# Kernel tuning notes

Hardware: AMD Instinct MI355X
Metric: run time of the kernel (lower is better)

Reference implementation:

```python
import jax, jax.numpy as jnp
import numpy as np

EMBED_DIM = 1024
HEAD_DIM = 64
BATCH = 2
SEQ = 4096


def setup_inputs() -> dict:
    key = jax.random.key(0)
    kx, kq, kk, kv = jax.random.split(key, 4)
    x = jax.random.normal(kx, (BATCH, SEQ, EMBED_DIM), dtype=jnp.float32)
    # nn.Linear(embedding_dim, head_dim, bias=False) weights, stored as [in, out]
    s = 1.0 / np.sqrt(EMBED_DIM)
    Wq = jax.random.uniform(kq, (EMBED_DIM, HEAD_DIM), jnp.float32, -s, s)
    Wk = jax.random.uniform(kk, (EMBED_DIM, HEAD_DIM), jnp.float32, -s, s)
    Wv = jax.random.uniform(kv, (EMBED_DIM, HEAD_DIM), jnp.float32, -s, s)
    return {"x": x, "Wq": Wq, "Wk": Wk, "Wv": Wv}


def reference(x, Wq, Wk, Wv):
    # x: [B, S, E]
    Q = x @ Wq  # [B, S, D]
    K = x @ Wk
    V = x @ Wv
    seq_len = Q.shape[1]
    head_dim = Q.shape[2]
    scores = jnp.einsum('bsd,btd->bst', Q, K) / jnp.sqrt(jnp.float32(head_dim))
    # Original adds a mask that is 1.0 on the causal (lower-tri) positions and
    # -inf elsewhere (tril(ones) with zeros replaced by -inf). The +1 on allowed
    # positions is a uniform row shift, but we keep it for bitwise faithfulness.
    causal = jnp.tril(jnp.ones((seq_len, seq_len), dtype=scores.dtype))
    mask = jnp.where(causal == 0, -jnp.inf, causal)
    scores = scores + mask  # [B, S, S]
    attn = jax.nn.softmax(scores, axis=-1)
    return jnp.einsum('bst,btd->bsd', attn, V)  # [B, S, D]
```

## Files before the change

### kernel.cpp

```cpp
#include <hip/hip_runtime.h>
#include <hip/hip_bf16.h>


typedef short short8 __attribute__((ext_vector_type(8)));
typedef float f32x4 __attribute__((ext_vector_type(4)));
typedef float f32x16 __attribute__((ext_vector_type(16)));
typedef unsigned int uint4e __attribute__((ext_vector_type(4)));
typedef unsigned short ushort4e __attribute__((ext_vector_type(4)));

#define NEGINF (-3.0e38f)
#define SCQ 0.18033688011112042f

static __device__ __forceinline__ unsigned short f2bf(float f) {
  __hip_bfloat16 h = __float2bfloat16(f);
  return __builtin_bit_cast(unsigned short, h);
}

static __device__ __forceinline__ f32x16 mfma32(short8 a, short8 b, f32x16 c) {
  return __builtin_amdgcn_mfma_f32_32x32x16_bf16(a, b, c, 0, 0, 0);
}

__global__ __launch_bounds__(256) void wprep_kernel(
    const float* __restrict__ Wq, const float* __restrict__ Wk,
    const float* __restrict__ Wv, unsigned short* __restrict__ Wt) {
  int w = blockIdx.x >> 3;
  int kc = blockIdx.x & 7;
  int k0 = kc * 128;
  const float* W = (w == 0) ? Wq : ((w == 1) ? Wk : Wv);
  float sc = (w == 0) ? SCQ : 1.0f;

  __shared__ unsigned short lt[128][66];
#pragma unroll
  for (int i = 0; i < 32; ++i) {
    int e = i * 256 + threadIdx.x;
    int k = e >> 6, n = e & 63;
    lt[k][n] = f2bf(W[(size_t)(k0 + k) * 64 + n] * sc);
  }
  __syncthreads();
#pragma unroll
  for (int i = 0; i < 32; ++i) {
    int e = i * 256 + threadIdx.x;
    int n = e >> 7, k = e & 127;
    Wt[(size_t)(w * 64 + n) * 1024 + k0 + k] = lt[k][n];
  }
}

__global__ __launch_bounds__(256, 2) void qkv_proj_kernel(
    const float* __restrict__ x, const unsigned short* __restrict__ Wt,
    unsigned short* __restrict__ Qb, unsigned short* __restrict__ Kb,
    unsigned short* __restrict__ Vt) {
  int lane = threadIdx.x & 63;
  int w = threadIdx.x >> 6;
  int r = lane & 15;
  int hi = lane >> 4;
  int sbase = blockIdx.x * 16;

  __shared__ alignas(16) float lds_part[4][3072];

  const float* xp = x + (size_t)(sbase + r) * 1024 + w * 256 + hi * 8;

  f32x4 acc[12];
#pragma unroll
  for (int t = 0; t < 12; ++t)
#pragma unroll
    for (int i = 0; i < 4; ++i) acc[t][i] = 0.f;

  f32x4 a0 = *(const f32x4*)(xp);
  f32x4 a1 = *(const f32x4*)(xp + 4);
#pragma unroll
  for (int k0 = 0; k0 < 256; k0 += 32) {
    short8 af;
#pragma unroll
    for (int j = 0; j < 4; ++j) {
      af[j] = (short)f2bf(a0[j]);
      af[4 + j] = (short)f2bf(a1[j]);
    }
    if (k0 + 32 < 256) {
      a0 = *(const f32x4*)(xp + k0 + 32);
      a1 = *(const f32x4*)(xp + k0 + 36);
    }
    const unsigned short* wb = Wt + (size_t)r * 1024 + w * 256 + k0 + hi * 8;
#pragma unroll
    for (int t = 0; t < 12; ++t) {
      short8 bf = *(const short8*)(wb + (size_t)((t >> 2) * 64 + (t & 3) * 16) * 1024);
      acc[t] = __builtin_amdgcn_mfma_f32_16x16x32_bf16(af, bf, acc[t], 0, 0, 0);
    }
  }

  float* lp = lds_part[w];
#pragma unroll
  for (int t = 0; t < 12; ++t)
#pragma unroll
    for (int v = 0; v < 4; ++v)
      lp[t * 256 + (hi * 4 + v) * 16 + r] = acc[t][v];
  __syncthreads();

#pragma unroll
  for (int i = 0; i < 2; ++i) {
    int task = threadIdx.x + i * 256;
    int t = task >> 6;
    int off = (task & 63) * 4;
    f32x4 s = *(const f32x4*)(&lds_part[0][t * 256 + off]);
    s += *(const f32x4*)(&lds_part[1][t * 256 + off]);
    s += *(const f32x4*)(&lds_part[2][t * 256 + off]);
    s += *(const f32x4*)(&lds_part[3][t * 256 + off]);
    int row = off >> 4, c0 = off & 15;
    ushort4e pk;
#pragma unroll
    for (int j = 0; j < 4; ++j) pk[j] = f2bf(s[j]);
    unsigned short* dst = (t < 4) ? Qb : Kb;
    *(ushort4e*)(dst + (size_t)(sbase + row) * 64 + (t & 3) * 16 + c0) = pk;
  }
  {
    int t = 8 + (threadIdx.x >> 6);
    int col = (threadIdx.x >> 2) & 15;
    int rg = threadIdx.x & 3;
    ushort4e pk;
#pragma unroll
    for (int j = 0; j < 4; ++j) {
      int idx = t * 256 + (rg * 4 + j) * 16 + col;
      float s = lds_part[0][idx] + lds_part[1][idx] + lds_part[2][idx] + lds_part[3][idx];
      pk[j] = f2bf(s);
    }
    int d = (t - 8) * 16 + col;
    int bidx = sbase >> 12, so = sbase & 4095;
    *(ushort4e*)(Vt + ((size_t)(bidx * 64 + d)) * 4096 + so + rg * 4) = pk;
  }
}

__global__ __launch_bounds__(512, 2) void attn_kernel(
    const unsigned short* __restrict__ Qb, const unsigned short* __restrict__ Kb,
    const unsigned short* __restrict__ Vt, float* __restrict__ out) {
  int qglob = blockIdx.x;
  int b = qglob >> 7;
  int q = qglob & 127;
  int lane = threadIdx.x & 63;
  int p = threadIdx.x >> 6;
  int ql = lane & 31;
  int h = lane >> 5;
  int sbase = q * 32;

  __shared__ float sm[8][32];
  __shared__ float sl[8][32];
  __shared__ alignas(16) float Op[8][32][68];

  const unsigned short* Qp = Qb + ((size_t)(b * 4096 + sbase + ql)) * 64 + h * 8;
  short8 qf0 = *(const short8*)(Qp);
  short8 qf1 = *(const short8*)(Qp + 16);
  short8 qf2 = *(const short8*)(Qp + 32);
  short8 qf3 = *(const short8*)(Qp + 48);

  f32x16 o0, o1;
#pragma unroll
  for (int i = 0; i < 16; ++i) { o0[i] = 0.f; o1[i] = 0.f; }
  float m = NEGINF, l = 0.f;

  int npairs = (q + 2) >> 1;
  const unsigned short* Kbb = Kb + (size_t)b * 4096 * 64;
  const unsigned short* Vbb = Vt + ((size_t)(b * 64 + ql)) * 4096 + h * 8;

  short8 k0a, k0b, k0c, k0d, k1a, k1b, k1c, k1d;
  {
    const unsigned short* Kp = Kbb + (size_t)(p * 64 + ql) * 64 + h * 8;
    k0a = *(const short8*)(Kp);
    k0b = *(const short8*)(Kp + 16);
    k0c = *(const short8*)(Kp + 32);
    k0d = *(const short8*)(Kp + 48);
    k1a = *(const short8*)(Kp + 2048);
    k1b = *(const short8*)(Kp + 2048 + 16);
    k1c = *(const short8*)(Kp + 2048 + 32);
    k1d = *(const short8*)(Kp + 2048 + 48);
  }

  for (int j = p; j < npairs; j += 8) {
    int kbase = j * 64;
    const unsigned short* Vp = Vbb + kbase;
    short8 vf0 = *(const short8*)(Vp);
    short8 vf1 = *(const short8*)(Vp + 16);
    short8 vf2 = *(const short8*)(Vp + 32);
    short8 vf3 = *(const short8*)(Vp + 48);
    short8 vg0 = *(const short8*)(Vp + 32 * 4096);
    short8 vg1 = *(const short8*)(Vp + 32 * 4096 + 16);
    short8 vg2 = *(const short8*)(Vp + 32 * 4096 + 32);
    short8 vg3 = *(const short8*)(Vp + 32 * 4096 + 48);

    f32x16 st0, st1;
#pragma unroll
    for (int i = 0; i < 16; ++i) { st0[i] = 0.f; st1[i] = 0.f; }
    st0 = mfma32(k0a, qf0, st0);
    st0 = mfma32(k0b, qf1, st0);
    st0 = mfma32(k0c, qf2, st0);
    st0 = mfma32(k0d, qf3, st0);
    st1 = mfma32(k1a, qf0, st1);
    st1 = mfma32(k1b, qf1, st1);
    st1 = mfma32(k1c, qf2, st1);
    st1 = mfma32(k1d, qf3, st1);

    if (j + 8 < npairs) {
      const unsigned short* Kp = Kbb + (size_t)((j + 8) * 64 + ql) * 64 + h * 8;
      k0a = *(const short8*)(Kp);
      k0b = *(const short8*)(Kp + 16);
      k0c = *(const short8*)(Kp + 32);
      k0d = *(const short8*)(Kp + 48);
      k1a = *(const short8*)(Kp + 2048);
      k1b = *(const short8*)(Kp + 2048 + 16);
      k1c = *(const short8*)(Kp + 2048 + 32);
      k1d = *(const short8*)(Kp + 2048 + 48);
    }

    if (2 * j == q) {
#pragma unroll
      for (int rg = 0; rg < 16; ++rg) {
        int kvl = (rg & 3) + 8 * (rg >> 2) + 4 * h;
        if (kvl > ql) st0[rg] = NEGINF;
        st1[rg] = NEGINF;
      }
    } else if (2 * j + 1 == q) {
#pragma unroll
      for (int rg = 0; rg < 16; ++rg) {
        int kvl = (rg & 3) + 8 * (rg >> 2) + 4 * h;
        if (kvl > ql) st1[rg] = NEGINF;
      }
    }

    float mx[16];
#pragma unroll
    for (int i = 0; i < 16; ++i) mx[i] = fmaxf(st0[i], st1[i]);
#pragma unroll
    for (int s = 8; s >= 1; s >>= 1)
#pragma unroll
      for (int i = 0; i < s; ++i) mx[i] = fmaxf(mx[i], mx[i + s]);
    float tm = fmaxf(mx[0], __shfl_xor(mx[0], 32));
    float nm = fmaxf(m, tm);
    float alpha = exp2f(m - nm);
#pragma unroll
    for (int i = 0; i < 16; ++i) {
      st0[i] = exp2f(st0[i] - nm);
      st1[i] = exp2f(st1[i] - nm);
    }
    float sv[16];
#pragma unroll
    for (int i = 0; i < 16; ++i) sv[i] = st0[i] + st1[i];
#pragma unroll
    for (int s = 8; s >= 1; s >>= 1)
#pragma unroll
      for (int i = 0; i < s; ++i) sv[i] += sv[i + s];
    float sum = sv[0] + __shfl_xor(sv[0], 32);
    l = l * alpha + sum;
    m = nm;
#pragma unroll
    for (int i = 0; i < 16; ++i) { o0[i] *= alpha; o1[i] *= alpha; }

    unsigned int pw0[8], pw1[8], sw0[8], sw1[8];
#pragma unroll
    for (int t = 0; t < 8; ++t) {
      pw0[t] = (unsigned int)f2bf(st0[2 * t]) | ((unsigned int)f2bf(st0[2 * t + 1]) << 16);
      pw1[t] = (unsigned int)f2bf(st1[2 * t]) | ((unsigned int)f2bf(st1[2 * t + 1]) << 16);
    }
#pragma unroll
    for (int t = 0; t < 8; ++t) {
      sw0[t] = __shfl_xor(pw0[t], 32);
      sw1[t] = __shfl_xor(pw1[t], 32);
    }
    uint4e bw0 = {h ? sw0[2] : pw0[0], h ? sw0[3] : pw0[1], h ? pw0[2] : sw0[0], h ? pw0[3] : sw0[1]};
    uint4e bw1 = {h ? sw0[6] : pw0[4], h ? sw0[7] : pw0[5], h ? pw0[6] : sw0[4], h ? pw0[7] : sw0[5]};
    uint4e bw2 = {h ? sw1[2] : pw1[0], h ? sw1[3] : pw1[1], h ? pw1[2] : sw1[0], h ? pw1[3] : sw1[1]};
    uint4e bw3 = {h ? sw1[6] : pw1[4], h ? sw1[7] : pw1[5], h ? pw1[6] : sw1[4], h ? pw1[7] : sw1[5]};
    short8 pb0 = __builtin_bit_cast(short8, bw0);
    short8 pb1 = __builtin_bit_cast(short8, bw1);
    short8 pb2 = __builtin_bit_cast(short8, bw2);
    short8 pb3 = __builtin_bit_cast(short8, bw3);

    o0 = mfma32(vf0, pb0, o0);
    o0 = mfma32(vf1, pb1, o0);
    o0 = mfma32(vf2, pb2, o0);
    o0 = mfma32(vf3, pb3, o0);
    o1 = mfma32(vg0, pb0, o1);
    o1 = mfma32(vg1, pb1, o1);
    o1 = mfma32(vg2, pb2, o1);
    o1 = mfma32(vg3, pb3, o1);
  }

  if (h == 0) sm[p][ql] = m;
  __syncthreads();
  float gm = sm[0][ql];
#pragma unroll
  for (int i = 1; i < 8; ++i) gm = fmaxf(gm, sm[i][ql]);
  float alpha = exp2f(m - gm);
  if (h == 0) sl[p][ql] = alpha * l;
  float* Ob = &Op[p][ql][0];
#pragma unroll
  for (int u = 0; u < 4; ++u) {
    f32x4 w0 = {alpha * o0[4 * u], alpha * o0[4 * u + 1], alpha * o0[4 * u + 2], alpha * o0[4 * u + 3]};
    *(f32x4*)(Ob + u * 8 + h * 4) = w0;
    f32x4 w1 = {alpha * o1[4 * u], alpha * o1[4 * u + 1], alpha * o1[4 * u + 2], alpha * o1[4 * u + 3]};
    *(f32x4*)(Ob + 32 + u * 8 + h * 4) = w1;
  }
  __syncthreads();

  int row = threadIdx.x >> 4;
  int c4 = (threadIdx.x & 15) * 4;
  f32x4 accv = *(const f32x4*)(&Op[0][row][c4]);
#pragma unroll
  for (int pp = 1; pp < 8; ++pp) accv += *(const f32x4*)(&Op[pp][row][c4]);
  float lsum = sl[0][row];
#pragma unroll
  for (int pp = 1; pp < 8; ++pp) lsum += sl[pp][row];
  float invl = 1.0f / lsum;
  f32x4 res;
#pragma unroll
  for (int j = 0; j < 4; ++j) res[j] = accv[j] * invl;
  *(f32x4*)(out + ((size_t)(b * 4096 + sbase + row)) * 64 + c4) = res;
}

extern "C" void kernel_launch(void* const* d_in, const int* in_sizes, int n_in,
                              void* d_out, int out_size, void* d_ws, size_t ws_size,
                              hipStream_t stream) {
  const float* x  = (const float*)d_in[0];
  const float* Wq = (const float*)d_in[1];
  const float* Wk = (const float*)d_in[2];
  const float* Wv = (const float*)d_in[3];
  float* out = (float*)d_out;

  if (ws_size < 3538944) return;

  char* ws = (char*)d_ws;
  unsigned short* Wt = (unsigned short*)(ws + 0);
  unsigned short* Qb = (unsigned short*)(ws + 393216);
  unsigned short* Kb = (unsigned short*)(ws + 1441792);
  unsigned short* Vt = (unsigned short*)(ws + 2490368);

  wprep_kernel<<<24, 256, 0, stream>>>(Wq, Wk, Wv, Wt);
  qkv_proj_kernel<<<512, 256, 0, stream>>>(x, Wt, Qb, Kb, Vt);
  attn_kernel<<<256, 512, 0, stream>>>(Qb, Kb, Vt, out);
}
```

Baseline: 134.1 us.

## Split attention KV range across four blocks with a separate combine kernel

The attention kernel now launches 1024 blocks of 256 threads instead of 256 blocks of 512. Each q-tile's KV pairs are split across four blocks (16 wave-groups total), and block order is reversed so the heaviest causal tiles run first. Partial outputs, maxes and sums go to workspace, and a new combine kernel merges them. The goal is better load balance and GPU occupancy on the causal workload. It adds an extra kernel launch plus about 8 MB of partial writes and reads. s_setprio hints are also placed around the MFMA blocks.

```diff
diff --git a/kernel.cpp b/kernel.cpp
--- a/kernel.cpp
+++ b/kernel.cpp
@@ -15,7 +15,6 @@
   __hip_bfloat16 h = __float2bfloat16(f);
   return __builtin_bit_cast(unsigned short, h);
 }
-
 static __device__ __forceinline__ f32x16 mfma32(short8 a, short8 b, f32x16 c) {
   return __builtin_amdgcn_mfma_f32_32x32x16_bf16(a, b, c, 0, 0, 0);
 }
@@ -128,21 +127,24 @@
   }
 }
 
-__global__ __launch_bounds__(512, 2) void attn_kernel(
+__global__ __launch_bounds__(256, 2) void attn_kernel(
     const unsigned short* __restrict__ Qb, const unsigned short* __restrict__ Kb,
-    const unsigned short* __restrict__ Vt, float* __restrict__ out) {
-  int qglob = blockIdx.x;
-  int b = qglob >> 7;
-  int q = qglob & 127;
+    const unsigned short* __restrict__ Vt, float* __restrict__ Opart,
+    float* __restrict__ Mpart, float* __restrict__ Lpart) {
+  int bid = blockIdx.x;
+  int q = 127 - (bid >> 3);
+  int b = (bid >> 2) & 1;
+  int hh = bid & 3;
   int lane = threadIdx.x & 63;
   int p = threadIdx.x >> 6;
+  int g = hh * 4 + p;
   int ql = lane & 31;
   int h = lane >> 5;
   int sbase = q * 32;
 
-  __shared__ float sm[8][32];
-  __shared__ float sl[8][32];
-  __shared__ alignas(16) float Op[8][32][68];
+  __shared__ float sm[4][32];
+  __shared__ float sl[4][32];
+  __shared__ alignas(16) float Op[4][32][68];
 
   const unsigned short* Qp = Qb + ((size_t)(b * 4096 + sbase + ql)) * 64 + h * 8;
   short8 qf0 = *(const short8*)(Qp);
@@ -161,7 +163,7 @@
 
   short8 k0a, k0b, k0c, k0d, k1a, k1b, k1c, k1d;
   {
-    const unsigned short* Kp = Kbb + (size_t)(p * 64 + ql) * 64 + h * 8;
+    const unsigned short* Kp = Kbb + (size_t)(g * 64 + ql) * 64 + h * 8;
     k0a = *(const short8*)(Kp);
     k0b = *(const short8*)(Kp + 16);
     k0c = *(const short8*)(Kp + 32);
@@ -172,7 +174,7 @@
     k1d = *(const short8*)(Kp + 2048 + 48);
   }
 
-  for (int j = p; j < npairs; j += 8) {
+  for (int j = g; j < npairs; j += 16) {
     int kbase = j * 64;
     const unsigned short* Vp = Vbb + kbase;
     short8 vf0 = *(const short8*)(Vp);
@@ -187,6 +189,7 @@
     f32x16 st0, st1;
 #pragma unroll
     for (int i = 0; i < 16; ++i) { st0[i] = 0.f; st1[i] = 0.f; }
+    __builtin_amdgcn_s_setprio(1);
     st0 = mfma32(k0a, qf0, st0);
     st0 = mfma32(k0b, qf1, st0);
     st0 = mfma32(k0c, qf2, st0);
@@ -195,9 +198,10 @@
     st1 = mfma32(k1b, qf1, st1);
     st1 = mfma32(k1c, qf2, st1);
     st1 = mfma32(k1d, qf3, st1);
-
-    if (j + 8 < npairs) {
-      const unsigned short* Kp = Kbb + (size_t)((j + 8) * 64 + ql) * 64 + h * 8;
+    __builtin_amdgcn_s_setprio(0);
+
+    if (j + 16 < npairs) {
+      const unsigned short* Kp = Kbb + (size_t)((j + 16) * 64 + ql) * 64 + h * 8;
       k0a = *(const short8*)(Kp);
       k0b = *(const short8*)(Kp + 16);
       k0c = *(const short8*)(Kp + 32);
@@ -271,6 +275,7 @@
     short8 pb2 = __builtin_bit_cast(short8, bw2);
     short8 pb3 = __builtin_bit_cast(short8, bw3);
 
+    __builtin_amdgcn_s_setprio(1);
     o0 = mfma32(vf0, pb0, o0);
     o0 = mfma32(vf1, pb1, o0);
     o0 = mfma32(vf2, pb2, o0);
@@ -279,13 +284,14 @@
     o1 = mfma32(vg1, pb1, o1);
     o1 = mfma32(vg2, pb2, o1);
     o1 = mfma32(vg3, pb3, o1);
+    __builtin_amdgcn_s_setprio(0);
   }
 
   if (h == 0) sm[p][ql] = m;
   __syncthreads();
   float gm = sm[0][ql];
 #pragma unroll
-  for (int i = 1; i < 8; ++i) gm = fmaxf(gm, sm[i][ql]);
+  for (int i = 1; i < 4; ++i) gm = fmaxf(gm, sm[i][ql]);
   float alpha = exp2f(m - gm);
   if (h == 0) sl[p][ql] = alpha * l;
   float* Ob = &Op[p][ql][0];
@@ -298,19 +304,55 @@
   }
   __syncthreads();
 
-  int row = threadIdx.x >> 4;
-  int c4 = (threadIdx.x & 15) * 4;
-  f32x4 accv = *(const f32x4*)(&Op[0][row][c4]);
-#pragma unroll
-  for (int pp = 1; pp < 8; ++pp) accv += *(const f32x4*)(&Op[pp][row][c4]);
-  float lsum = sl[0][row];
-#pragma unroll
-  for (int pp = 1; pp < 8; ++pp) lsum += sl[pp][row];
-  float invl = 1.0f / lsum;
-  f32x4 res;
-#pragma unroll
-  for (int j = 0; j < 4; ++j) res[j] = accv[j] * invl;
-  *(f32x4*)(out + ((size_t)(b * 4096 + sbase + row)) * 64 + c4) = res;
+  float* Od = Opart + (size_t)bid * 2048;
+#pragma unroll
+  for (int i = 0; i < 2; ++i) {
+    int task = threadIdx.x + i * 256;
+    int row = task >> 4;
+    int c4 = (task & 15) * 4;
+    f32x4 accv = *(const f32x4*)(&Op[0][row][c4]);
+#pragma unroll
+    for (int pp = 1; pp < 4; ++pp) accv += *(const f32x4*)(&Op[pp][row][c4]);
+    *(f32x4*)(Od + row * 64 + c4) = accv;
+  }
+  if (threadIdx.x < 32) {
+    int row = threadIdx.x;
+    float gmv = fmaxf(fmaxf(sm[0][row], sm[1][row]), fmaxf(sm[2][row], sm[3][row]));
+    Mpart[(size_t)bid * 32 + row] = gmv;
+    Lpart[(size_t)bid * 32 + row] = sl[0][row] + sl[1][row] + sl[2][row] + sl[3][row];
+  }
+}
+
+__global__ __launch_bounds__(256) void combine_kernel(
+    const float* __restrict__ Opart, const float* __restrict__ Mpart,
+    const float* __restrict__ Lpart, float* __restrict__ out) {
+  int gid = blockIdx.x * 256 + threadIdx.x;
+  int c4 = (gid & 15) * 4;
+  int row = gid >> 4;
+  int r = row & 31;
+  int qg = row >> 5;
+  int b = qg >> 7, q = qg & 127;
+  int base = (127 - q) * 8 + b * 4;
+
+  float mm[4];
+  float gm = NEGINF;
+#pragma unroll
+  for (int i = 0; i < 4; ++i) {
+    mm[i] = Mpart[(size_t)(base + i) * 32 + r];
+    gm = fmaxf(gm, mm[i]);
+  }
+  float L = 0.f;
+  f32x4 o = {0.f, 0.f, 0.f, 0.f};
+#pragma unroll
+  for (int i = 0; i < 4; ++i) {
+    float e = exp2f(mm[i] - gm);
+    L += e * Lpart[(size_t)(base + i) * 32 + r];
+    f32x4 ov = *(const f32x4*)(Opart + (size_t)(base + i) * 2048 + r * 64 + c4);
+    o += e * ov;
+  }
+  float invl = 1.0f / L;
+  f32x4 res = {o[0] * invl, o[1] * invl, o[2] * invl, o[3] * invl};
+  *(f32x4*)(out + (size_t)row * 64 + c4) = res;
 }
 
 extern "C" void kernel_launch(void* const* d_in, const int* in_sizes, int n_in,
@@ -322,15 +364,19 @@
   const float* Wv = (const float*)d_in[3];
   float* out = (float*)d_out;
 
-  if (ws_size < 3538944) return;
+  if (ws_size < 12189696) return;
 
   char* ws = (char*)d_ws;
   unsigned short* Wt = (unsigned short*)(ws + 0);
   unsigned short* Qb = (unsigned short*)(ws + 393216);
   unsigned short* Kb = (unsigned short*)(ws + 1441792);
   unsigned short* Vt = (unsigned short*)(ws + 2490368);
+  float* Opart = (float*)(ws + 3538944);
+  float* Mpart = (float*)(ws + 11927552);
+  float* Lpart = (float*)(ws + 12058624);
 
   wprep_kernel<<<24, 256, 0, stream>>>(Wq, Wk, Wv, Wt);
   qkv_proj_kernel<<<512, 256, 0, stream>>>(x, Wt, Qb, Kb, Vt);
-  attn_kernel<<<256, 512, 0, stream>>>(Qb, Kb, Vt, out);
-}
+  attn_kernel<<<1024, 256, 0, stream>>>(Qb, Kb, Vt, Opart, Mpart, Lpart);
+  combine_kernel<<<512, 256, 0, stream>>>(Opart, Mpart, Lpart, out);
+}
```

Result: faster. 128.1 us (-4.5%).
